# Optimization experiments

Hardware: AMD Instinct MI355X
Metric: run time of the kernel (lower is better)

The kernel has to match this reference:

```python
import jax, jax.numpy as jnp
import numpy as np

B, D, H, W, C = 8, 4, 56, 56, 128
HEADS = 4
WD, WH, WW = 2, 7, 7
SD, SH, SW = 1, 3, 3
N = WD * WH * WW            # tokens per window = 98
NW = (D // WD) * (H // WH) * (W // WW)  # windows per sample = 128
SCALE = (C // HEADS) ** -0.5
EPS = 1e-5


def _rel_pos_index():
    coords = np.stack(np.meshgrid(np.arange(WD), np.arange(WH), np.arange(WW), indexing='ij'))
    coords = coords.reshape(3, -1)                    # (3, N)
    rel = (coords[:, :, None] - coords[:, None, :]).transpose(1, 2, 0)  # (N, N, 3)
    rel[:, :, 0] += WD - 1
    rel[:, :, 1] += WH - 1
    rel[:, :, 2] += WW - 1
    rel[:, :, 0] *= (2 * WH - 1) * (2 * WW - 1)
    rel[:, :, 1] *= (2 * WW - 1)
    return rel.sum(-1)                                # (N, N) int

REL_IDX = jnp.asarray(_rel_pos_index())


def _np_window_partition(x, wd, wh, ww):
    b, d, h, w, c = x.shape
    x = x.reshape(b, d // wd, wd, h // wh, wh, w // ww, ww, c)
    return x.transpose(0, 1, 3, 5, 2, 4, 6, 7).reshape(-1, wd * wh * ww, c)


def _attn_mask():
    img = np.zeros((1, D, H, W, 1), np.float32)
    cnt = 0
    for ds in (slice(None, -WD), slice(-WD, -SD), slice(-SD, None)):
        for hs in (slice(None, -WH), slice(-WH, -SH), slice(-SH, None)):
            for ws in (slice(None, -WW), slice(-WW, -SW), slice(-SW, None)):
                img[:, ds, hs, ws, :] = cnt
                cnt += 1
    mw = _np_window_partition(img, WD, WH, WW)[..., 0]         # (nW, N)
    m = mw[:, None, :] - mw[:, :, None]                        # (nW, N, N)
    return jnp.asarray(np.where(m != 0, -100.0, 0.0).astype(np.float32))

ATTN_MASK = _attn_mask()  # (nW, N, N)


def window_partition(x):
    b = x.shape[0]
    x = x.reshape(b, D // WD, WD, H // WH, WH, W // WW, WW, C)
    return x.transpose(0, 1, 3, 5, 2, 4, 6, 7).reshape(-1, N, C)


def window_reverse(wins, b):
    x = wins.reshape(b, D // WD, H // WH, W // WW, WD, WH, WW, C)
    return x.transpose(0, 1, 4, 2, 5, 3, 6, 7).reshape(b, D, H, W, C)


def layernorm(x, g, b):
    mu = jnp.mean(x, axis=-1, keepdims=True)
    var = jnp.mean(jnp.square(x - mu), axis=-1, keepdims=True)
    return (x - mu) / jnp.sqrt(var + EPS) * g + b


def swin_block(x, norm1_g, norm1_b, qkv_w, qkv_b, rpb_table, proj_w, proj_b,
               norm2_g, norm2_b, fc1_w, fc1_b, fc2_w, fc2_b):
    shortcut = x
    h1 = layernorm(x, norm1_g, norm1_b)
    # cyclic shift (pad amounts are 0 for these dims)
    shifted = jnp.roll(h1, (-SD, -SH, -SW), axis=(1, 2, 3))
    xw = window_partition(shifted)                    # (B*nW, N, C)
    Bn = xw.shape[0]
    qkv = (xw @ qkv_w + qkv_b).reshape(Bn, N, 3, HEADS, C // HEADS)
    qkv = qkv.transpose(2, 0, 3, 1, 4)                # (3, Bn, h, N, c)
    q, k, v = qkv[0], qkv[1], qkv[2]
    attn = jnp.einsum('bhnc,bhmc->bhnm', q * SCALE, k)
    bias = rpb_table[REL_IDX].transpose(2, 0, 1)      # (h, N, N)
    attn = attn + bias[None]
    attn = attn.reshape(B, NW, HEADS, N, N) + ATTN_MASK[None, :, None]
    attn = jax.nn.softmax(attn.reshape(Bn, HEADS, N, N), axis=-1)
    out = jnp.einsum('bhnm,bhmc->bhnc', attn, v)
    out = out.transpose(0, 2, 1, 3).reshape(Bn, N, C)
    out = out @ proj_w + proj_b
    xr = window_reverse(out, B)
    xr = jnp.roll(xr, (SD, SH, SW), axis=(1, 2, 3))
    x1 = shortcut + xr
    h2 = layernorm(x1, norm2_g, norm2_b)
    mlp = jax.nn.gelu(h2 @ fc1_w + fc1_b, approximate=False) @ fc2_w + fc2_b
    return x1 + mlp


def setup_inputs() -> dict:
    key = jax.random.key(0)
    ks = jax.random.split(key, 6)
    s = 0.02
    return {
        'x': jax.random.normal(ks[0], (B, D, H, W, C), jnp.float32),
        'norm1_g': jnp.ones((C,), jnp.float32),
        'norm1_b': jnp.zeros((C,), jnp.float32),
        'qkv_w': jax.random.normal(ks[1], (C, 3 * C), jnp.float32) * s,
        'qkv_b': jnp.zeros((3 * C,), jnp.float32),
        'rpb_table': jax.random.normal(ks[2], ((2 * WD - 1) * (2 * WH - 1) * (2 * WW - 1), HEADS), jnp.float32) * s,
        'proj_w': jax.random.normal(ks[3], (C, C), jnp.float32) * s,
        'proj_b': jnp.zeros((C,), jnp.float32),
        'norm2_g': jnp.ones((C,), jnp.float32),
        'norm2_b': jnp.zeros((C,), jnp.float32),
        'fc1_w': jax.random.normal(ks[4], (C, 4 * C), jnp.float32) * s,
        'fc1_b': jnp.zeros((4 * C,), jnp.float32),
        'fc2_w': jax.random.normal(ks[5], (4 * C, C), jnp.float32) * s,
        'fc2_b': jnp.zeros((C,), jnp.float32),
    }


def reference(x, norm1_g, norm1_b, qkv_w, qkv_b, rpb_table, proj_w, proj_b,
              norm2_g, norm2_b, fc1_w, fc1_b, fc2_w, fc2_b):
    return swin_block(x, norm1_g, norm1_b, qkv_w, qkv_b, rpb_table, proj_w, proj_b,
                      norm2_g, norm2_b, fc1_w, fc1_b, fc2_w, fc2_b)
```

## Files before the change

### kernel.cpp

```cpp
#include <hip/hip_runtime.h>
#include <hip/hip_bf16.h>
#include <cstdint>
#include <cstddef>

using bf16 = __hip_bfloat16;
typedef __bf16 bf16x8 __attribute__((ext_vector_type(8)));
typedef float f32x4 __attribute__((ext_vector_type(4)));

#define DEV static __device__ __forceinline__

DEV bf16 f2b(float x) { return __float2bfloat16(x); }
DEV float b2f(bf16 x) { return __bfloat162float(x); }
DEV f32x4 mfma16(bf16x8 a, bf16x8 b, f32x4 c) {
    return __builtin_amdgcn_mfma_f32_16x16x32_bf16(a, b, c, 0, 0, 0);
}
DEV float gelu_f(float x) {
    float u2 = x * x;
    float u = x * (0.7978845608028654f + 0.0356774081363001f * u2);
    float s = 1.f / (1.f + __expf(-2.f * u));
    return x * s;
}
DEV void gload16(const bf16* g, bf16* l) {
    __builtin_amdgcn_global_load_lds(
        (const __attribute__((address_space(1))) unsigned int*)g,
        (__attribute__((address_space(3))) unsigned int*)l, 16, 0, 0);
}

constexpr int NTOK = 98;
constexpr int BNWIN = 1024;
constexpr int MTOT = BNWIN * NTOK;
constexpr float SCALE = 0.17677669529663687f;
constexpr float EPS = 1e-5f;

__global__ __launch_bounds__(256) void k_prep(const float* __restrict__ qkv_w,
        const float* __restrict__ proj_w, const float* __restrict__ fc1_w,
        const float* __restrict__ fc2_w, const float* __restrict__ rpb,
        bf16* __restrict__ QWs, bf16* __restrict__ PW,
        bf16* __restrict__ W1, bf16* __restrict__ W2, float* __restrict__ BM) {
    int tid = blockIdx.x * 256 + threadIdx.x;
    int stride = gridDim.x * 256;
    for (int i = tid; i < 384 * 128; i += stride) {
        int t = i >> 13, r = (i >> 7) & 63, kswz = i & 127;
        int k = kswz ^ ((r & 7) << 3);
        QWs[i] = f2b(qkv_w[(size_t)k * 384 + t * 64 + r]);
    }
    for (int i = tid; i < 128 * 128; i += stride) {
        int n = i >> 7, k = i & 127;
        PW[i] = f2b(proj_w[k * 128 + n]);
    }
    for (int i = tid; i < 512 * 128; i += stride) {
        int t = i >> 13, r = (i >> 7) & 63, kswz = i & 127;
        int k = kswz ^ ((r & 7) << 3);
        W1[i] = f2b(fc1_w[(size_t)k * 512 + t * 64 + r]);
    }
    for (int i = tid; i < 512 * 128; i += stride) {
        int t = i >> 13, c = (i >> 6) & 127, kswz = i & 63;
        int kk = kswz ^ ((c & 7) << 3);
        W2[i] = f2b(fc2_w[(size_t)(t * 64 + kk) * 128 + c]);
    }
    for (int i = tid; i < 8 * 4 * 98 * 98; i += stride) {
        int cls = i / 38416, r = i - cls * 38416;
        int h = r / 9604, r2 = r - h * 9604;
        int ii = r2 / 98, jj = r2 - ii * 98;
        int di = ii >= 49, ri = ii - di * 49, hi = ri / 7, wi = ri - hi * 7;
        int dj = jj >= 49, rj = jj - dj * 49, hj = rj / 7, wj = rj - hj * 7;
        int bidx = (di - dj + 1) * 169 + (hi - hj + 6) * 13 + (wi - wj + 6);
        int db = cls >> 2, hb7 = (cls >> 1) & 1, wb7 = cls & 1;
        int ti = (db ? 1 + di : 0) * 9 + (hb7 ? (hi < 4 ? 1 : 2) : 0) * 3
               + (wb7 ? (wi < 4 ? 1 : 2) : 0);
        int tj = (db ? 1 + dj : 0) * 9 + (hb7 ? (hj < 4 ? 1 : 2) : 0) * 3
               + (wb7 ? (wj < 4 ? 1 : 2) : 0);
        BM[i] = rpb[bidx * 4 + h] + ((ti != tj) ? -100.f : 0.f);
    }
}

__global__ __launch_bounds__(256) void k_qkvln(const float* __restrict__ x,
        const float* __restrict__ g, const float* __restrict__ be,
        const bf16* __restrict__ QWs, const float* __restrict__ bias,
        bf16* __restrict__ out) {
    __shared__ __align__(16) bf16 As[64 * 136];
    __shared__ __align__(16) bf16 Bt[64 * 128];
    int tid = threadIdx.x;
    int row0 = blockIdx.x * 64;
    int wave = tid >> 6, lane = tid & 63;
    int lrow = lane & 15, kg8 = (lane >> 4) * 8, g4 = (lane >> 4) * 4;
    int swzq = (lrow & 7) << 3;

    #pragma unroll
    for (int p = 0; p < 4; ++p) {
        int vi = tid + p * 256;
        int row = vi >> 4, cg = vi & 15;
        int r = row0 + row;
        int bn = r / 98, n = r - bn * 98;
        int b = bn >> 7, wr = bn & 127;
        int dB = wr >> 6, hB = (wr >> 3) & 7, wB = wr & 7;
        int dd = (n >= 49), rem = n - dd * 49;
        int hh = rem / 7, ww = rem - hh * 7;
        int dp = dB * 2 + dd, hp = hB * 7 + hh, wp = wB * 7 + ww;
        int ds = (dp + 1) & 3;
        int hs = hp + 3; if (hs >= 56) hs -= 56;
        int wsv = wp + 3; if (wsv >= 56) wsv -= 56;
        size_t src = ((size_t)((b * 4 + ds) * 56 + hs) * 56 + wsv) * 128 + cg * 8;
        float4 v0 = *(const float4*)&x[src];
        float4 v1 = *(const float4*)&x[src + 4];
        float s = v0.x + v0.y + v0.z + v0.w + v1.x + v1.y + v1.z + v1.w;
        float sq = v0.x*v0.x + v0.y*v0.y + v0.z*v0.z + v0.w*v0.w
                 + v1.x*v1.x + v1.y*v1.y + v1.z*v1.z + v1.w*v1.w;
        #pragma unroll
        for (int m = 1; m < 16; m <<= 1) { s += __shfl_xor(s, m); sq += __shfl_xor(sq, m); }
        float mean = s * (1.f / 128.f);
        float var = sq * (1.f / 128.f) - mean * mean;
        float rstd = rsqrtf(var + EPS);
        float4 g0 = *(const float4*)&g[cg * 8], g1 = *(const float4*)&g[cg * 8 + 4];
        float4 e0 = *(const float4*)&be[cg * 8], e1 = *(const float4*)&be[cg * 8 + 4];
        union { bf16x8 v8; bf16 h[8]; } o;
        o.h[0] = f2b((v0.x - mean) * rstd * g0.x + e0.x);
        o.h[1] = f2b((v0.y - mean) * rstd * g0.y + e0.y);
        o.h[2] = f2b((v0.z - mean) * rstd * g0.z + e0.z);
        o.h[3] = f2b((v0.w - mean) * rstd * g0.w + e0.w);
        o.h[4] = f2b((v1.x - mean) * rstd * g1.x + e1.x);
        o.h[5] = f2b((v1.y - mean) * rstd * g1.y + e1.y);
        o.h[6] = f2b((v1.z - mean) * rstd * g1.z + e1.z);
        o.h[7] = f2b((v1.w - mean) * rstd * g1.w + e1.w);
        *(bf16x8*)&As[row * 136 + cg * 8] = o.v8;
    }
    __syncthreads();

    bf16x8 a1[4];
    #pragma unroll
    for (int ksi = 0; ksi < 4; ++ksi)
        a1[ksi] = *(const bf16x8*)&As[(wave * 16 + lrow) * 136 + ksi * 32 + kg8];

    for (int c6 = 0; c6 < 6; ++c6) {
        const bf16* Bg = QWs + c6 * 8192;
        #pragma unroll
        for (int j = 0; j < 4; ++j) {
            int chunk = wave * 4 + j;
            gload16(Bg + chunk * 512 + lane * 8, Bt + chunk * 512);
        }
        __syncthreads();

        f32x4 acc[4] = {};
        #pragma unroll
        for (int ksi = 0; ksi < 4; ++ksi) {
            int k0 = ksi * 32 + kg8;
            #pragma unroll
            for (int ct = 0; ct < 4; ++ct) {
                bf16x8 bb = *(const bf16x8*)&Bt[(ct * 16 + lrow) * 128 + (k0 ^ swzq)];
                acc[ct] = mfma16(a1[ksi], bb, acc[ct]);
            }
        }
        #pragma unroll
        for (int ct = 0; ct < 4; ++ct) {
            int gcol = c6 * 64 + ct * 16 + lrow;
            float bv = bias[gcol];
            #pragma unroll
            for (int r2 = 0; r2 < 4; ++r2) {
                int grow = row0 + wave * 16 + g4 + r2;
                out[(size_t)grow * 384 + gcol] = f2b(acc[ct][r2] + bv);
            }
        }
        __syncthreads();
    }
}

__global__ __launch_bounds__(256) void k_attn(const bf16* __restrict__ qkv,
        const float* __restrict__ BM, bf16* __restrict__ aout) {
    __shared__ __align__(16) bf16 qs[112 * 40];
    __shared__ __align__(16) bf16 ksm[112 * 40];
    __shared__ __align__(16) bf16 vt[32 * 136];
    __shared__ __align__(16) bf16 ps[64 * 136];

    int tid = threadIdx.x;
    int bn = blockIdx.x, h = blockIdx.y;
    int wrw = bn & 127;
    int cls = ((wrw >> 6) << 2) | (((((wrw >> 3) & 7) == 7) ? 1 : 0) << 1)
            | (((wrw & 7) == 7) ? 1 : 0);
    const float* bmbase = &BM[((size_t)cls * 4 + h) * 9604];

    {
        uint32_t* z1 = (uint32_t*)qs;
        uint32_t* z2 = (uint32_t*)ksm;
        for (int i = tid; i < 2240; i += 256) { z1[i] = 0u; z2[i] = 0u; }
        uint32_t* z3 = (uint32_t*)vt;
        for (int i = tid; i < 2176; i += 256) z3[i] = 0u;
        uint32_t* z4 = (uint32_t*)ps;
        for (int i = tid; i < 4352; i += 256) z4[i] = 0u;
    }
    __syncthreads();
    const size_t base = (size_t)bn * 98 * 384 + h * 32;
    for (int ch = tid; ch < 1176; ch += 256) {
        int mat = ch / 392;
        int rem = ch - mat * 392;
        int row = rem >> 2, cg = rem & 3;
        uint4 v = *(const uint4*)&qkv[base + (size_t)row * 384 + mat * 128 + cg * 8];
        if (mat == 0)      *(uint4*)&qs[row * 40 + cg * 8] = v;
        else if (mat == 1) *(uint4*)&ksm[row * 40 + cg * 8] = v;
        else {
            const bf16* pv = (const bf16*)&v;
            #pragma unroll
            for (int j = 0; j < 8; ++j) vt[(cg * 8 + j) * 136 + row] = pv[j];
        }
    }
    __syncthreads();

    int wave = tid >> 6, lane = tid & 63;
    int lrow = lane & 15, kg8 = (lane >> 4) * 8, g4 = (lane >> 4) * 4;

    for (int rt = wave; rt < 7; rt += 4) {
        f32x4 sacc[7];
        bf16x8 qa = *(const bf16x8*)&qs[(rt * 16 + lrow) * 40 + kg8];
        #pragma unroll
        for (int ct = 0; ct < 7; ++ct) {
            bf16x8 kb = *(const bf16x8*)&ksm[(ct * 16 + lrow) * 40 + kg8];
            f32x4 z = {};
            sacc[ct] = mfma16(qa, kb, z);
        }
        #pragma unroll
        for (int r2 = 0; r2 < 4; ++r2) {
            int grow = rt * 16 + g4 + r2;
            int mi = grow < 98 ? grow : 97;
            const float* btrow = &bmbase[mi * 98];
            float val[7];
            float mx = -1e30f;
            #pragma unroll
            for (int ct = 0; ct < 7; ++ct) {
                int jc = ct * 16 + lrow;
                int jj = jc < 98 ? jc : 97;
                float v = sacc[ct][r2] * SCALE + btrow[jj];
                if (jc >= 98) v = -1e30f;
                val[ct] = v;
                mx = fmaxf(mx, v);
            }
            #pragma unroll
            for (int m = 1; m < 16; m <<= 1) mx = fmaxf(mx, __shfl_xor(mx, m));
            float sum = 0.f;
            #pragma unroll
            for (int ct = 0; ct < 7; ++ct) { val[ct] = __expf(val[ct] - mx); sum += val[ct]; }
            #pragma unroll
            for (int m = 1; m < 16; m <<= 1) sum += __shfl_xor(sum, m);
            float inv = 1.f / sum;
            #pragma unroll
            for (int ct = 0; ct < 7; ++ct)
                ps[(wave * 16 + g4 + r2) * 136 + ct * 16 + lrow] = f2b(val[ct] * inv);
        }
        #pragma unroll
        for (int ct = 0; ct < 2; ++ct) {
            f32x4 oacc = {};
            #pragma unroll
            for (int ksi = 0; ksi < 4; ++ksi) {
                bf16x8 pa = *(const bf16x8*)&ps[(wave * 16 + lrow) * 136 + ksi * 32 + kg8];
                bf16x8 vb = *(const bf16x8*)&vt[(ct * 16 + lrow) * 136 + ksi * 32 + kg8];
                oacc = mfma16(pa, vb, oacc);
            }
            #pragma unroll
            for (int r2 = 0; r2 < 4; ++r2) {
                int grow = rt * 16 + g4 + r2;
                if (grow < 98)
                    aout[((size_t)bn * 98 + grow) * 128 + h * 32 + ct * 16 + lrow] =
                        f2b(oacc[r2]);
            }
        }
    }
}

__global__ __launch_bounds__(256) void k_proj(const bf16* __restrict__ A,
        const bf16* __restrict__ PW, const float* __restrict__ pb,
        const float* __restrict__ x, const float* __restrict__ g2,
        const float* __restrict__ be2,
        bf16* __restrict__ x1, bf16* __restrict__ h2) {
    __shared__ __align__(16) bf16 As[64 * 136];
    __shared__ __align__(16) bf16 Bt[128 * 136];
    int tid = threadIdx.x;
    int row0 = blockIdx.x * 64;
    #pragma unroll
    for (int p = 0; p < 4; ++p) {
        int vi = tid + p * 256;
        int row = vi >> 4, cg = vi & 15;
        *(uint4*)&As[row * 136 + cg * 8] =
            *(const uint4*)&A[(size_t)(row0 + row) * 128 + cg * 8];
    }
    #pragma unroll
    for (int p = 0; p < 8; ++p) {
        int vi = tid + p * 256;
        int row = vi >> 4, cg = vi & 15;
        *(uint4*)&Bt[row * 136 + cg * 8] =
            *(const uint4*)&PW[(size_t)row * 128 + cg * 8];
    }
    __syncthreads();
    int wave = tid >> 6, lane = tid & 63;
    int lrow = lane & 15, kg8 = (lane >> 4) * 8, g4 = (lane >> 4) * 4;
    f32x4 acc[8] = {};
    #pragma unroll
    for (int ksi = 0; ksi < 4; ++ksi) {
        bf16x8 a = *(const bf16x8*)&As[(wave * 16 + lrow) * 136 + ksi * 32 + kg8];
        #pragma unroll
        for (int ct = 0; ct < 8; ++ct) {
            bf16x8 bb = *(const bf16x8*)&Bt[(ct * 16 + lrow) * 136 + ksi * 32 + kg8];
            acc[ct] = mfma16(a, bb, acc[ct]);
        }
    }
    #pragma unroll
    for (int r2 = 0; r2 < 4; ++r2) {
        int rwin = row0 + wave * 16 + g4 + r2;
        int bn = rwin / 98, n = rwin - bn * 98;
        int b = bn >> 7, wr2 = bn & 127;
        int dB = wr2 >> 6, hB = (wr2 >> 3) & 7, wB = wr2 & 7;
        int dd = n >= 49, rem = n - dd * 49;
        int hh = rem / 7, ww2 = rem - hh * 7;
        int dp = dB * 2 + dd, hp = hB * 7 + hh, wp = wB * 7 + ww2;
        int d2 = (dp + 1) & 3;
        int hv = hp + 3; if (hv >= 56) hv -= 56;
        int wv = wp + 3; if (wv >= 56) wv -= 56;
        size_t dst = ((size_t)(b * 4 + d2) * 56 + hv) * 56 + wv;
        float vals[8], s = 0.f, sq = 0.f;
        #pragma unroll
        for (int ct = 0; ct < 8; ++ct) {
            int col = ct * 16 + lrow;
            float v = acc[ct][r2] + pb[col] + x[dst * 128 + col];
            vals[ct] = v; s += v; sq += v * v;
        }
        #pragma unroll
        for (int m = 1; m < 16; m <<= 1) { s += __shfl_xor(s, m); sq += __shfl_xor(sq, m); }
        float mean = s * (1.f / 128.f);
        float var = sq * (1.f / 128.f) - mean * mean;
        float rstd = rsqrtf(var + EPS);
        #pragma unroll
        for (int ct = 0; ct < 8; ++ct) {
            int col = ct * 16 + lrow;
            x1[dst * 128 + col] = f2b(vals[ct]);
            h2[dst * 128 + col] = f2b((vals[ct] - mean) * rstd * g2[col] + be2[col]);
        }
    }
}

__global__ __launch_bounds__(512) void k_mlp(const bf16* __restrict__ h2,
        const bf16* __restrict__ W1s, const float* __restrict__ b1,
        const bf16* __restrict__ W2s, const float* __restrict__ b2v,
        const bf16* __restrict__ x1, float* __restrict__ out) {
    __shared__ __align__(16) bf16 W1b[8192];
    __shared__ __align__(16) bf16 W2b[8192];
    __shared__ __align__(16) bf16 Ts[128 * 72];
    int tid = threadIdx.x;
    int row0 = blockIdx.x * 128;
    int wave = tid >> 6, lane = tid & 63;
    int lrow = lane & 15, kg8 = (lane >> 4) * 8, g4 = (lane >> 4) * 4;
    int swz = (lrow & 7) << 3;

    bf16x8 a1[4];
    const bf16* arow = &h2[(size_t)(row0 + wave * 16 + lrow) * 128];
    #pragma unroll
    for (int ksi = 0; ksi < 4; ++ksi)
        a1[ksi] = *(const bf16x8*)&arow[ksi * 32 + kg8];

    f32x4 oacc[8] = {};
    for (int hc = 0; hc < 8; ++hc) {
        const bf16* W1g = W1s + hc * 8192;
        const bf16* W2g = W2s + hc * 8192;
        #pragma unroll
        for (int j = 0; j < 4; ++j) {
            int chunk = wave + j * 8;
            if (chunk < 16) gload16(W1g + chunk * 512 + lane * 8, W1b + chunk * 512);
            else            gload16(W2g + (chunk - 16) * 512 + lane * 8, W2b + (chunk - 16) * 512);
        }
        __syncthreads();

        f32x4 tacc[4] = {};
        #pragma unroll
        for (int ksi = 0; ksi < 4; ++ksi) {
            int k0 = ksi * 32 + kg8;
            #pragma unroll
            for (int ct = 0; ct < 4; ++ct) {
                bf16x8 bb = *(const bf16x8*)&W1b[(ct * 16 + lrow) * 128 + (k0 ^ swz)];
                tacc[ct] = mfma16(a1[ksi], bb, tacc[ct]);
            }
        }
        #pragma unroll
        for (int ct = 0; ct < 4; ++ct) {
            int hcol = hc * 64 + ct * 16 + lrow;
            float bb = b1[hcol];
            #pragma unroll
            for (int r2 = 0; r2 < 4; ++r2) {
                float t = gelu_f(tacc[ct][r2] + bb);
                Ts[(wave * 16 + g4 + r2) * 72 + ct * 16 + lrow] = f2b(t);
            }
        }
        #pragma unroll
        for (int ksi = 0; ksi < 2; ++ksi) {
            int k0 = ksi * 32 + kg8;
            bf16x8 a = *(const bf16x8*)&Ts[(wave * 16 + lrow) * 72 + k0];
            #pragma unroll
            for (int ct = 0; ct < 8; ++ct) {
                bf16x8 bb = *(const bf16x8*)&W2b[(ct * 16 + lrow) * 64 + (k0 ^ swz)];
                oacc[ct] = mfma16(a, bb, oacc[ct]);
            }
        }
        __syncthreads();
    }
    #pragma unroll
    for (int ct = 0; ct < 8; ++ct) {
        int col = ct * 16 + lrow;
        float bb = b2v[col];
        #pragma unroll
        for (int r2 = 0; r2 < 4; ++r2) {
            size_t grow = (size_t)row0 + wave * 16 + g4 + r2;
            out[grow * 128 + col] = oacc[ct][r2] + bb + b2f(x1[grow * 128 + col]);
        }
    }
}

extern "C" void kernel_launch(void* const* d_in, const int* in_sizes, int n_in,
                              void* d_out, int out_size, void* d_ws, size_t ws_size,
                              hipStream_t stream) {
    (void)in_sizes; (void)n_in; (void)out_size; (void)ws_size;
    const float* x      = (const float*)d_in[0];
    const float* n1g    = (const float*)d_in[1];
    const float* n1b    = (const float*)d_in[2];
    const float* qkv_w  = (const float*)d_in[3];
    const float* qkv_b  = (const float*)d_in[4];
    const float* rpb    = (const float*)d_in[5];
    const float* proj_w = (const float*)d_in[6];
    const float* proj_b = (const float*)d_in[7];
    const float* n2g    = (const float*)d_in[8];
    const float* n2b    = (const float*)d_in[9];
    const float* fc1_w  = (const float*)d_in[10];
    const float* fc1_b  = (const float*)d_in[11];
    const float* fc2_w  = (const float*)d_in[12];
    const float* fc2_b  = (const float*)d_in[13];
    float* outp = (float*)d_out;

    char* ws = (char*)d_ws;
    constexpr size_t S = (size_t)MTOT * 128 * 2;
    bf16*  qkvbuf = (bf16*)(ws + S);
    bf16*  aout   = (bf16*)ws;
    bf16*  x1     = (bf16*)(ws + S);
    bf16*  h2     = (bf16*)(ws + 3 * S);
    char* wp_ = ws + 4 * S;
    bf16*  QWs = (bf16*)wp_;
    bf16*  PW  = (bf16*)(wp_ + 98304);
    bf16*  W1s = (bf16*)(wp_ + 98304 + 32768);
    bf16*  W2s = (bf16*)(wp_ + 98304 + 32768 + 131072);
    float* BMb = (float*)(wp_ + 98304 + 32768 + 131072 + 131072);

    k_prep <<<192, 256, 0, stream>>>(qkv_w, proj_w, fc1_w, fc2_w, rpb, QWs, PW, W1s, W2s, BMb);
    k_qkvln<<<MTOT / 64, 256, 0, stream>>>(x, n1g, n1b, QWs, qkv_b, qkvbuf);
    k_attn <<<dim3(BNWIN, 4), 256, 0, stream>>>(qkvbuf, BMb, aout);
    k_proj <<<MTOT / 64, 256, 0, stream>>>(aout, PW, proj_b, x, n2g, n2b, x1, h2);
    k_mlp  <<<MTOT / 128, 512, 0, stream>>>(h2, W1s, fc1_b, W2s, fc2_b, x1, outp);
}
```

Baseline: 195.1 us.

## Store QKV in per-head contiguous layout and async-load Q/K into LDS

The QKV GEMM epilogue now writes its output in a [window][mat][head][token][32] layout instead of row-major 384-wide rows. The attention kernel can then read each head's Q and K as contiguous 6272-byte blocks using global_load_lds DMA into unpadded LDS tiles, and read V contiguously. This cuts strided global reads and the zero-fill of the Q/K tiles. In exchange, the GEMM stores become scattered 2-byte writes with a 64-byte stride, and dropping the padded 40-element LDS stride may cause bank conflicts on Q/K fragment reads.

```diff
diff --git a/kernel.cpp b/kernel.cpp
--- a/kernel.cpp
+++ b/kernel.cpp
@@ -152,12 +152,17 @@
         }
         #pragma unroll
         for (int ct = 0; ct < 4; ++ct) {
-            int gcol = c6 * 64 + ct * 16 + lrow;
-            float bv = bias[gcol];
+            int gcol = c6 * 64 + ct * 16;
+            int mat = gcol >> 7;
+            int head = (gcol >> 5) & 3;
+            int cb = gcol & 31;
+            float bv = bias[gcol + lrow];
+            size_t mb = (size_t)(mat * 4 + head) * 3136 + cb + lrow;
             #pragma unroll
             for (int r2 = 0; r2 < 4; ++r2) {
                 int grow = row0 + wave * 16 + g4 + r2;
-                out[(size_t)grow * 384 + gcol] = f2b(acc[ct][r2] + bv);
+                int bn = grow / 98, n = grow - bn * 98;
+                out[(size_t)bn * 37632 + mb + n * 32] = f2b(acc[ct][r2] + bv);
             }
         }
         __syncthreads();
@@ -166,8 +171,8 @@
 
 __global__ __launch_bounds__(256) void k_attn(const bf16* __restrict__ qkv,
         const float* __restrict__ BM, bf16* __restrict__ aout) {
-    __shared__ __align__(16) bf16 qs[112 * 40];
-    __shared__ __align__(16) bf16 ksm[112 * 40];
+    __shared__ __align__(16) bf16 qs[112 * 32];
+    __shared__ __align__(16) bf16 ksm[112 * 32];
     __shared__ __align__(16) bf16 vt[32 * 136];
     __shared__ __align__(16) bf16 ps[64 * 136];
 
@@ -179,28 +184,28 @@
     const float* bmbase = &BM[((size_t)cls * 4 + h) * 9604];
 
     {
-        uint32_t* z1 = (uint32_t*)qs;
-        uint32_t* z2 = (uint32_t*)ksm;
-        for (int i = tid; i < 2240; i += 256) { z1[i] = 0u; z2[i] = 0u; }
+        uint32_t* z1 = (uint32_t*)(qs + 98 * 32);
+        uint32_t* z2 = (uint32_t*)(ksm + 98 * 32);
+        for (int i = tid; i < 224; i += 256) { z1[i] = 0u; z2[i] = 0u; }
         uint32_t* z3 = (uint32_t*)vt;
         for (int i = tid; i < 2176; i += 256) z3[i] = 0u;
         uint32_t* z4 = (uint32_t*)ps;
         for (int i = tid; i < 4352; i += 256) z4[i] = 0u;
     }
     __syncthreads();
-    const size_t base = (size_t)bn * 98 * 384 + h * 32;
-    for (int ch = tid; ch < 1176; ch += 256) {
-        int mat = ch / 392;
-        int rem = ch - mat * 392;
-        int row = rem >> 2, cg = rem & 3;
-        uint4 v = *(const uint4*)&qkv[base + (size_t)row * 384 + mat * 128 + cg * 8];
-        if (mat == 0)      *(uint4*)&qs[row * 40 + cg * 8] = v;
-        else if (mat == 1) *(uint4*)&ksm[row * 40 + cg * 8] = v;
-        else {
-            const bf16* pv = (const bf16*)&v;
-            #pragma unroll
-            for (int j = 0; j < 8; ++j) vt[(cg * 8 + j) * 136 + row] = pv[j];
-        }
+    const bf16* qg = qkv + (size_t)(bn * 12 + h) * 3136;
+    const bf16* kg = qkv + (size_t)(bn * 12 + 4 + h) * 3136;
+    const bf16* vg = qkv + (size_t)(bn * 12 + 8 + h) * 3136;
+    for (int i = tid; i < 392; i += 256) {
+        gload16(qg + i * 8, qs + i * 8);
+        gload16(kg + i * 8, ksm + i * 8);
+    }
+    for (int i = tid; i < 392; i += 256) {
+        uint4 v = *(const uint4*)&vg[i * 8];
+        int n = i >> 2, c0 = (i & 3) * 8;
+        const bf16* pv = (const bf16*)&v;
+        #pragma unroll
+        for (int j = 0; j < 8; ++j) vt[(c0 + j) * 136 + n] = pv[j];
     }
     __syncthreads();
 
@@ -209,10 +214,10 @@
 
     for (int rt = wave; rt < 7; rt += 4) {
         f32x4 sacc[7];
-        bf16x8 qa = *(const bf16x8*)&qs[(rt * 16 + lrow) * 40 + kg8];
+        bf16x8 qa = *(const bf16x8*)&qs[(rt * 16 + lrow) * 32 + kg8];
         #pragma unroll
         for (int ct = 0; ct < 7; ++ct) {
-            bf16x8 kb = *(const bf16x8*)&ksm[(ct * 16 + lrow) * 40 + kg8];
+            bf16x8 kb = *(const bf16x8*)&ksm[(ct * 16 + lrow) * 32 + kg8];
             f32x4 z = {};
             sacc[ct] = mfma16(qa, kb, z);
         }
```

New measurement: 203.4 us. 4.3% more time.
